# Kernel tuning notes

Measured on AMD Instinct MI355X. Metric: run time of the kernel, lower is better.

The kernel has to match this reference:

```python
import jax, jax.numpy as jnp
import numpy as np

EPS_EIGH = 1e-07
B, D = 16384, 64


def setup_inputs() -> dict:
    key = jax.random.key(0)
    A = jax.random.normal(key, (B, D, D), dtype=jnp.float32)
    # SPD construction: A A^T / D + eps*I -> positive, well-separated eigenvalues
    X = jnp.einsum('bij,bkj->bik', A, A) / D + 1e-3 * jnp.eye(D, dtype=jnp.float32)
    return {"X": X}


def reference(X):
    # symmetrize (matches 0.5*(X + X^T) in the torch forward)
    Xs = 0.5 * (X + jnp.swapaxes(X, -1, -2))
    eigvals, eigvecs = jnp.linalg.eigh(Xs)          # (B, D), (B, D, D)
    log_eigvals = jnp.log(jnp.clip(eigvals, EPS_EIGH, None))
    # U diag(log(lambda)) U^T, without materializing diag_embed
    return jnp.einsum('bij,bj,bkj->bik', eigvecs, log_eigvals, eigvecs)
```

## Files before the change

kernel.cpp:

```cpp
#include <hip/hip_runtime.h>
#include <math.h>

#define DD 64
#define NSWEEP 7

typedef float f32x2 __attribute__((ext_vector_type(2)));

__device__ __forceinline__ float rdlane(float v, int l) {
    return __int_as_float(__builtin_amdgcn_readlane(__float_as_int(v), l));
}
__device__ __forceinline__ float bperm(int paddr, float v) {
    return __int_as_float(__builtin_amdgcn_ds_bpermute(paddr, __float_as_int(v)));
}

__global__ __launch_bounds__(64, 2)
void logeig_sweeps_kernel(const float* __restrict__ X, float* __restrict__ Wout, int nb) {
    const int b = blockIdx.x;
    if (b >= nb) return;
    const int lane = threadIdx.x & 63;
    const float* Xb = X + (size_t)b * DD * DD;

    f32x2 w2[DD / 2];
    #pragma unroll
    for (int i = 0; i < DD / 2; ++i) {
        const int e0 = 2 * i, e1 = 2 * i + 1;
        w2[i].x = 0.5f * (Xb[e0 * DD + lane] + Xb[lane * DD + e0]);
        w2[i].y = 0.5f * (Xb[e1 * DD + lane] + Xb[lane * DD + e1]);
    }

    #pragma unroll
    for (int k = 0; k < DD; ++k) {
        const float pivot = rdlane(w2[k >> 1][k & 1], k);
        const float rinv  = 1.0f / sqrtf(pivot);
        const float ljk   = w2[k >> 1][k & 1] * rinv;
        const bool  gtk   = (lane > k);
        const bool  eqk   = (lane == k);
        #pragma unroll
        for (int e = k; e < DD; ++e) {
            const float we  = w2[e >> 1][e & 1];
            const float lek = rdlane(we, k) * rinv;
            const float upd = fmaf(-lek, ljk, we);
            w2[e >> 1][e & 1] = eqk ? lek : (gtk ? upd : we);
        }
    }
    #pragma unroll
    for (int e = 0; e < DD - 1; ++e)
        if (e < lane) w2[e >> 1][e & 1] = 0.0f;

    float nown;
    {
        f32x2 nv0 = {0.f, 0.f}, nv1 = {0.f, 0.f};
        #pragma unroll
        for (int i = 0; i < DD / 2; i += 2) {
            nv0 = w2[i] * w2[i] + nv0;
            nv1 = w2[i + 1] * w2[i + 1] + nv1;
        }
        nown = (nv0.x + nv0.y) + (nv1.x + nv1.y);
    }

    const int lane4 = lane << 2;

    for (int sw = 0; sw < NSWEEP; ++sw) {
        bool sweep_rotated = false;
        for (int m = 1; m < DD; ++m) {
            const int paddr = lane4 ^ (m << 2);

            f32x2 oth2[DD / 2];
            #pragma unroll
            for (int i = 0; i < DD / 2; ++i) {
                oth2[i].x = bperm(paddr, w2[i].x);
                oth2[i].y = bperm(paddr, w2[i].y);
            }

            f32x2 dv0 = {0.f, 0.f}, dv1 = {0.f, 0.f};
            #pragma unroll
            for (int i = 0; i < DD / 2; i += 2) {
                dv0 = w2[i] * oth2[i] + dv0;
                dv1 = w2[i + 1] * oth2[i + 1] + dv1;
            }
            const float d    = (dv0.x + dv0.y) + (dv1.x + dv1.y);
            const float noth = bperm(paddr, nown);

            const bool dorot = (d * d > 1e-8f * nown * noth);
            if (__any(dorot)) {
                sweep_rotated = true;
                const bool  islo = (paddr > lane4);
                const float app  = islo ? nown : noth;
                const float aqq  = islo ? noth : nown;
                float tau = (aqq - app) * 0.5f / d;
                float t   = 1.0f / (fabsf(tau) + sqrtf(fmaf(tau, tau, 1.0f)));
                t = copysignf(t, tau);
                float c = 1.0f / sqrtf(fmaf(t, t, 1.0f));
                float s = t * c;
                float tsgn = islo ? -t : t;
                if (!islo) s = -s;
                if (!dorot) { c = 1.0f; s = 0.0f; tsgn = 0.0f; }
                nown = fmaf(tsgn, d, nown);

                const f32x2 c2 = {c, c};
                const f32x2 s2 = {s, s};
                #pragma unroll
                for (int i = 0; i < DD / 2; ++i)
                    w2[i] = c2 * w2[i] - s2 * oth2[i];
            }
        }
        if (!sweep_rotated) break;
    }

    float* Wb = Wout + (size_t)b * DD * DD;
    #pragma unroll
    for (int e = 0; e < DD; ++e)
        Wb[e * DD + lane] = w2[e >> 1][e & 1];
}

__global__ __launch_bounds__(256, 2)
void logeig_epilogue_kernel(float* __restrict__ out, int nb) {
    __shared__ float M[DD][DD + 1];
    __shared__ float sc[DD];

    const int b = blockIdx.x;
    if (b >= nb) return;
    const int tid  = threadIdx.x;
    const int lane = tid & 63;
    const int w4   = tid >> 6;
    float* Ob = out + (size_t)b * DD * DD;

    #pragma unroll
    for (int ii = 0; ii < 16; ++ii) {
        int r = w4 * 16 + ii;
        M[r][lane] = Ob[r * DD + lane];
    }
    __syncthreads();

    if (tid < DD) {
        float n0 = 0.f, n1 = 0.f;
        #pragma unroll
        for (int e = 0; e < DD; e += 2) {
            n0 = fmaf(M[e][tid],     M[e][tid],     n0);
            n1 = fmaf(M[e + 1][tid], M[e + 1][tid], n1);
        }
        const float nn = n0 + n1;
        sc[tid] = logf(fmaxf(nn, 1e-7f)) / nn;
    }
    __syncthreads();

    float vrow[DD];
    #pragma unroll
    for (int j = 0; j < DD; ++j) vrow[j] = M[lane][j] * sc[j];

    float acc[16];
    #pragma unroll
    for (int ii = 0; ii < 16; ++ii) acc[ii] = 0.0f;

    for (int k = 0; k < DD; ++k) {
        const float vl = vrow[k];
        #pragma unroll
        for (int ii = 0; ii < 16; ++ii)
            acc[ii] = fmaf(M[w4 * 16 + ii][k], vl, acc[ii]);
    }

    __syncthreads();
    #pragma unroll
    for (int ii = 0; ii < 16; ++ii)
        Ob[(size_t)(w4 * 16 + ii) * DD + lane] = acc[ii];
}

extern "C" void kernel_launch(void* const* d_in, const int* in_sizes, int n_in,
                              void* d_out, int out_size, void* d_ws, size_t ws_size,
                              hipStream_t stream) {
    (void)n_in; (void)d_ws; (void)ws_size; (void)out_size;
    const float* X = (const float*)d_in[0];
    float* out = (float*)d_out;
    int nb = in_sizes[0] / (DD * DD);
    hipLaunchKernelGGL(logeig_sweeps_kernel, dim3(nb), dim3(DD), 0, stream, X, out, nb);
    hipLaunchKernelGGL(logeig_epilogue_kernel, dim3(nb), dim3(256), 0, stream, out, nb);
}
```

Before: 5.158 ms.

## Split one-sided Jacobi rows across two wavefronts with LDS dot-product reduction

The Jacobi sweep kernel now runs two wavefronts per matrix. Each wavefront holds half of every column (32 rows) in registers and does half the bpermute, dot-product and rotation work. Partial dot products and norms are combined through double-buffered shared memory with a __syncthreads per pair step. This halves per-wave register pressure and serial work, at the cost of a block barrier every pair iteration and a Cholesky stage that both waves compute redundantly.

```diff
diff --git a/kernel.cpp b/kernel.cpp
--- a/kernel.cpp
+++ b/kernel.cpp
@@ -13,73 +13,86 @@
     return __int_as_float(__builtin_amdgcn_ds_bpermute(paddr, __float_as_int(v)));
 }
 
-__global__ __launch_bounds__(64, 2)
+__global__ __launch_bounds__(128, 2)
 void logeig_sweeps_kernel(const float* __restrict__ X, float* __restrict__ Wout, int nb) {
+    __shared__ float hd[2][2][DD];
+    __shared__ float hn[2][DD];
+
     const int b = blockIdx.x;
     if (b >= nb) return;
-    const int lane = threadIdx.x & 63;
+    const int tid  = threadIdx.x;
+    const int lane = tid & 63;
+    const int h    = tid >> 6;
     const float* Xb = X + (size_t)b * DD * DD;
 
-    f32x2 w2[DD / 2];
+    float w[DD];
     #pragma unroll
-    for (int i = 0; i < DD / 2; ++i) {
-        const int e0 = 2 * i, e1 = 2 * i + 1;
-        w2[i].x = 0.5f * (Xb[e0 * DD + lane] + Xb[lane * DD + e0]);
-        w2[i].y = 0.5f * (Xb[e1 * DD + lane] + Xb[lane * DD + e1]);
-    }
+    for (int e = 0; e < DD; ++e)
+        w[e] = 0.5f * (Xb[e * DD + lane] + Xb[lane * DD + e]);
 
     #pragma unroll
     for (int k = 0; k < DD; ++k) {
-        const float pivot = rdlane(w2[k >> 1][k & 1], k);
+        const float pivot = rdlane(w[k], k);
         const float rinv  = 1.0f / sqrtf(pivot);
-        const float ljk   = w2[k >> 1][k & 1] * rinv;
+        const float ljk   = w[k] * rinv;
         const bool  gtk   = (lane > k);
         const bool  eqk   = (lane == k);
         #pragma unroll
         for (int e = k; e < DD; ++e) {
-            const float we  = w2[e >> 1][e & 1];
-            const float lek = rdlane(we, k) * rinv;
-            const float upd = fmaf(-lek, ljk, we);
-            w2[e >> 1][e & 1] = eqk ? lek : (gtk ? upd : we);
+            const float lek = rdlane(w[e], k) * rinv;
+            const float upd = fmaf(-lek, ljk, w[e]);
+            w[e] = eqk ? lek : (gtk ? upd : w[e]);
         }
     }
     #pragma unroll
     for (int e = 0; e < DD - 1; ++e)
-        if (e < lane) w2[e >> 1][e & 1] = 0.0f;
+        if (e < lane) w[e] = 0.0f;
 
-    float nown;
-    {
-        f32x2 nv0 = {0.f, 0.f}, nv1 = {0.f, 0.f};
-        #pragma unroll
-        for (int i = 0; i < DD / 2; i += 2) {
-            nv0 = w2[i] * w2[i] + nv0;
-            nv1 = w2[i + 1] * w2[i + 1] + nv1;
-        }
-        nown = (nv0.x + nv0.y) + (nv1.x + nv1.y);
+    f32x2 w2[16];
+    #pragma unroll
+    for (int i = 0; i < 16; ++i) {
+        w2[i].x = w[h * 32 + 2 * i];
+        w2[i].y = w[h * 32 + 2 * i + 1];
     }
 
+    {
+        f32x2 a0 = {0.f, 0.f}, a1 = {0.f, 0.f};
+        #pragma unroll
+        for (int i = 0; i < 16; i += 2) {
+            a0 = w2[i] * w2[i] + a0;
+            a1 = w2[i + 1] * w2[i + 1] + a1;
+        }
+        hn[h][lane] = (a0.x + a0.y) + (a1.x + a1.y);
+    }
+    __syncthreads();
+    float nown = hn[0][lane] + hn[1][lane];
+
     const int lane4 = lane << 2;
+    int g = 0;
 
     for (int sw = 0; sw < NSWEEP; ++sw) {
         bool sweep_rotated = false;
-        for (int m = 1; m < DD; ++m) {
+        for (int m = 1; m < DD; ++m, ++g) {
             const int paddr = lane4 ^ (m << 2);
+            const int par   = g & 1;
 
-            f32x2 oth2[DD / 2];
+            f32x2 oth2[16];
             #pragma unroll
-            for (int i = 0; i < DD / 2; ++i) {
+            for (int i = 0; i < 16; ++i) {
                 oth2[i].x = bperm(paddr, w2[i].x);
                 oth2[i].y = bperm(paddr, w2[i].y);
             }
 
             f32x2 dv0 = {0.f, 0.f}, dv1 = {0.f, 0.f};
             #pragma unroll
-            for (int i = 0; i < DD / 2; i += 2) {
+            for (int i = 0; i < 16; i += 2) {
                 dv0 = w2[i] * oth2[i] + dv0;
                 dv1 = w2[i + 1] * oth2[i + 1] + dv1;
             }
-            const float d    = (dv0.x + dv0.y) + (dv1.x + dv1.y);
+            hd[par][h][lane] = (dv0.x + dv0.y) + (dv1.x + dv1.y);
             const float noth = bperm(paddr, nown);
+            __syncthreads();
+            const float d = hd[par][0][lane] + hd[par][1][lane];
 
             const bool dorot = (d * d > 1e-8f * nown * noth);
             if (__any(dorot)) {
@@ -100,7 +113,7 @@
                 const f32x2 c2 = {c, c};
                 const f32x2 s2 = {s, s};
                 #pragma unroll
-                for (int i = 0; i < DD / 2; ++i)
+                for (int i = 0; i < 16; ++i)
                     w2[i] = c2 * w2[i] - s2 * oth2[i];
             }
         }
@@ -109,8 +122,10 @@
 
     float* Wb = Wout + (size_t)b * DD * DD;
     #pragma unroll
-    for (int e = 0; e < DD; ++e)
-        Wb[e * DD + lane] = w2[e >> 1][e & 1];
+    for (int i = 0; i < 16; ++i) {
+        Wb[(h * 32 + 2 * i) * DD + lane]     = w2[i].x;
+        Wb[(h * 32 + 2 * i + 1) * DD + lane] = w2[i].y;
+    }
 }
 
 __global__ __launch_bounds__(256, 2)
@@ -172,6 +187,6 @@
     const float* X = (const float*)d_in[0];
     float* out = (float*)d_out;
     int nb = in_sizes[0] / (DD * DD);
-    hipLaunchKernelGGL(logeig_sweeps_kernel, dim3(nb), dim3(DD), 0, stream, X, out, nb);
+    hipLaunchKernelGGL(logeig_sweeps_kernel, dim3(nb), dim3(128), 0, stream, X, out, nb);
     hipLaunchKernelGGL(logeig_epilogue_kernel, dim3(nb), dim3(256), 0, stream, out, nb);
 }
```

Result: slower. 5.833 ms (+13.1%).
